# Performance work log

Hardware: AMD Instinct MI355X
Metric: run time of the kernel (lower is better)

## Reference

```python
import jax, jax.numpy as jnp
import numpy as np

NUM_EXPERT = 16
IN_FEAT = 1024
OUT_FEAT = 2048
N_TOKENS = 4096


def setup_inputs() -> dict:
    key = jax.random.key(0)
    k1, k2, k3 = jax.random.split(key, 3)
    x = jax.random.uniform(k1, (N_TOKENS, IN_FEAT), dtype=jnp.float32)
    gate = jax.random.randint(k2, (N_TOKENS,), 0, NUM_EXPERT, dtype=jnp.int32)
    # expert weights: [num_expert, out_feat, in_feat]
    weight = jax.random.normal(k3, (NUM_EXPERT, OUT_FEAT, IN_FEAT), dtype=jnp.float32) * 0.02
    return {"x": x, "gate": gate, "weight": weight}


def reference(x, gate, weight):
    # out[b] = weight[gate[b]] @ x[b]
    # Avoid materializing weight[gate] ([B, O, I] would be huge): scan over the
    # small, fixed expert axis with input masking (tokens not routed to expert e
    # contribute zero rows to that expert's GEMM).
    B = x.shape[0]
    E, O, I = weight.shape
    out0 = jnp.zeros((B, O), dtype=x.dtype)

    def body(out, ew):
        e, W = ew  # W: [O, I]
        xm = jnp.where((gate == e)[:, None], x, 0.0)  # [B, I] masked tokens
        return out + jnp.einsum("bi,oi->bo", xm, W), None

    out, _ = jax.lax.scan(body, out0, (jnp.arange(E), weight))
    return out
```

## Files before the change

kernel.cpp:

```cpp
#include <hip/hip_runtime.h>
#include <hip/hip_bf16.h>
#include <stdint.h>

#define N_TOKENS   4096
#define IN_FEAT    1024
#define OUT_FEAT   2048
#define NUM_EXPERT 16

#define BM 128
#define BN 128
#define BK 32
#define MAX_TILES 48
#define MAX_ROWS  6144

typedef __bf16 bf16x8 __attribute__((ext_vector_type(8)));
typedef float  f32x4  __attribute__((ext_vector_type(4)));
typedef unsigned short us8 __attribute__((ext_vector_type(8)));

__device__ __forceinline__ unsigned short f32_to_bf16_rne(float f) {
  union { float f; uint32_t u; } v; v.f = f;
  uint32_t u = v.u;
  u += 0x7fffu + ((u >> 16) & 1u);
  return (unsigned short)(u >> 16);
}

__device__ __forceinline__ void async_copy16(const void* g, void* l) {
  __builtin_amdgcn_global_load_lds(
      (const __attribute__((address_space(1))) unsigned int*)g,
      (__attribute__((address_space(3))) unsigned int*)l, 16, 0, 0);
}

__global__ void k_setup(const int* __restrict__ gate,
                        int* __restrict__ pstart,
                        int* __restrict__ tile_e,
                        int* __restrict__ tile_m,
                        int* __restrict__ row_token)
{
  __shared__ int cnt[NUM_EXPERT];
  __shared__ int cur[NUM_EXPERT];
  __shared__ int ps[NUM_EXPERT];
  const int tid = threadIdx.x;
  if (tid < NUM_EXPERT) { cnt[tid] = 0; cur[tid] = 0; }
  __syncthreads();
  for (int b = tid; b < N_TOKENS; b += 256) atomicAdd(&cnt[gate[b]], 1);
  for (int r = tid; r < MAX_ROWS; r += 256) row_token[r] = -1;
  __syncthreads();
  if (tid == 0) {
    int p = 0, tot = 0;
    for (int e = 0; e < NUM_EXPERT; ++e) {
      ps[e] = p; pstart[e] = p;
      int nt = (cnt[e] + BM - 1) / BM;
      for (int t = 0; t < nt; ++t) { tile_e[tot] = e; tile_m[tot] = t; ++tot; }
      p += nt * BM;
    }
    for (int s = tot; s < MAX_TILES; ++s) { tile_e[s] = -1; tile_m[s] = 0; }
  }
  __syncthreads();
  for (int b = tid; b < N_TOKENS; b += 256) {
    int e = gate[b];
    int pos = atomicAdd(&cur[e], 1);
    row_token[ps[e] + pos] = b;
  }
}

__global__ void k_gather_x(const float4* __restrict__ x,
                           const int* __restrict__ row_token,
                           us8* __restrict__ xs) {
  const int r = blockIdx.x * 2 + (threadIdx.x >> 7);
  const int c = threadIdx.x & 127;
  const int tok = row_token[r];
  us8 o;
  if (tok >= 0) {
    float4 a = x[tok * 256 + c * 2];
    float4 b = x[tok * 256 + c * 2 + 1];
    o[0] = f32_to_bf16_rne(a.x); o[1] = f32_to_bf16_rne(a.y);
    o[2] = f32_to_bf16_rne(a.z); o[3] = f32_to_bf16_rne(a.w);
    o[4] = f32_to_bf16_rne(b.x); o[5] = f32_to_bf16_rne(b.y);
    o[6] = f32_to_bf16_rne(b.z); o[7] = f32_to_bf16_rne(b.w);
  } else {
    o = (us8)0;
  }
  xs[r * 128 + c] = o;
}

__global__ void __launch_bounds__(256)
k_gemm(const unsigned short* __restrict__ xs,
       const float* __restrict__ w,
       const int* __restrict__ pstart,
       const int* __restrict__ tile_e,
       const int* __restrict__ tile_m,
       const int* __restrict__ row_token,
       float* __restrict__ out) {
  __shared__ us8   As[512];
  __shared__ f32x4 Bs[1024];
  __shared__ int rowtok_s[BM];

  const int slot = blockIdx.y;
  const int e = tile_e[slot];
  if (e < 0) return;
  const int seg0 = pstart[e] + tile_m[slot] * BM;
  const int n0 = blockIdx.x * BN;

  const int tid  = threadIdx.x;
  const int wid  = tid >> 6;
  const int lane = tid & 63;
  const int lr   = lane & 15;
  const int quad = lane >> 4;
  const int wm   = (wid >> 1) * 64;
  const int wn   = (wid & 1) * 64;

  if (tid < BM) rowtok_s[tid] = row_token[seg0 + tid];

  const int cA = (tid & 3) ^ ((tid >> 3) & 3);
  const int cB = (tid & 7) ^ ((tid >> 3) & 7);
  const unsigned short* agp = xs + (size_t)(seg0 + (tid >> 2)) * IN_FEAT + cA * 8;
  const float* bgp = w + (size_t)e * OUT_FEAT * IN_FEAT
                       + (size_t)(n0 + (tid >> 3)) * IN_FEAT + cB * 4;

  f32x4 acc[4][4];
  const f32x4 z = {0.f, 0.f, 0.f, 0.f};
#pragma unroll
  for (int i = 0; i < 4; ++i)
#pragma unroll
    for (int j = 0; j < 4; ++j) acc[i][j] = z;

  for (int k0 = 0; k0 < IN_FEAT; k0 += BK) {
    async_copy16(agp + k0,                 As + wid * 64);
    async_copy16(agp + 64 * IN_FEAT + k0,  As + 256 + wid * 64);
    async_copy16(bgp + k0,                 Bs + wid * 64);
    async_copy16(bgp + 32 * IN_FEAT + k0,  Bs + 256 + wid * 64);
    async_copy16(bgp + 64 * IN_FEAT + k0,  Bs + 512 + wid * 64);
    async_copy16(bgp + 96 * IN_FEAT + k0,  Bs + 768 + wid * 64);
    __syncthreads();

    bf16x8 af[4], bf[4];
#pragma unroll
    for (int mi = 0; mi < 4; ++mi) {
      const int n = wm + mi * 16 + lr;
      af[mi] = *(const bf16x8*)&As[n * 4 + (quad ^ ((n >> 1) & 3))];
    }
#pragma unroll
    for (int ni = 0; ni < 4; ++ni) {
      const int n = wn + ni * 16 + lr;
      f32x4 c0 = Bs[n * 8 + ((2 * quad)     ^ (n & 7))];
      f32x4 c1 = Bs[n * 8 + ((2 * quad + 1) ^ (n & 7))];
      bf16x8 b;
      b[0] = (__bf16)c0[0]; b[1] = (__bf16)c0[1];
      b[2] = (__bf16)c0[2]; b[3] = (__bf16)c0[3];
      b[4] = (__bf16)c1[0]; b[5] = (__bf16)c1[1];
      b[6] = (__bf16)c1[2]; b[7] = (__bf16)c1[3];
      bf[ni] = b;
    }
#pragma unroll
    for (int mi = 0; mi < 4; ++mi)
#pragma unroll
      for (int ni = 0; ni < 4; ++ni)
        acc[mi][ni] = __builtin_amdgcn_mfma_f32_16x16x32_bf16(
            af[mi], bf[ni], acc[mi][ni], 0, 0, 0);
    __syncthreads();
  }

#pragma unroll
  for (int mi = 0; mi < 4; ++mi) {
    const int mb = wm + mi * 16 + quad * 4;
    const int t0 = rowtok_s[mb + 0];
    const int t1 = rowtok_s[mb + 1];
    const int t2 = rowtok_s[mb + 2];
    const int t3 = rowtok_s[mb + 3];
#pragma unroll
    for (int ni = 0; ni < 4; ++ni) {
      const int n = n0 + wn + ni * 16 + lr;
      f32x4 c = acc[mi][ni];
      if (t0 >= 0) out[(size_t)t0 * OUT_FEAT + n] = c[0];
      if (t1 >= 0) out[(size_t)t1 * OUT_FEAT + n] = c[1];
      if (t2 >= 0) out[(size_t)t2 * OUT_FEAT + n] = c[2];
      if (t3 >= 0) out[(size_t)t3 * OUT_FEAT + n] = c[3];
    }
  }
}

extern "C" void kernel_launch(void* const* d_in, const int* in_sizes, int n_in,
                              void* d_out, int out_size, void* d_ws, size_t ws_size,
                              hipStream_t stream) {
  const float* x    = (const float*)d_in[0];
  const int*   gate = (const int*)d_in[1];
  const float* w    = (const float*)d_in[2];
  float* out = (float*)d_out;

  char* ws = (char*)d_ws;
  unsigned short* xs = (unsigned short*)ws;
  int* row_token = (int*)(ws + 12582912);
  int* pstart = row_token + MAX_ROWS;
  int* tile_e = pstart + NUM_EXPERT;
  int* tile_m = tile_e + MAX_TILES;

  k_setup<<<1, 256, 0, stream>>>(gate, pstart, tile_e, tile_m, row_token);
  k_gather_x<<<MAX_ROWS / 2, 256, 0, stream>>>((const float4*)x, row_token,
                                               (us8*)xs);
  dim3 g(OUT_FEAT / BN, MAX_TILES);
  k_gemm<<<g, 256, 0, stream>>>(xs, w, pstart, tile_e, tile_m, row_token, out);
}
```

Before: 260.5 us.

## Double-buffer LDS tiles in expert GEMM to overlap global loads with MFMA

The GEMM main loop now uses two LDS buffers for the A and B tiles. It issues the async global-to-LDS copies for the next K-step before computing on the current one, and waits with explicit vmcnt counts and raw s_barrier instead of __syncthreads. The goal is to hide global memory latency behind the bf16 MFMA work. The cost is double the shared memory, which can lower occupancy, and hand-written waitcnt logic that depends on the exact count of outstanding loads.

```diff
diff --git a/kernel.cpp b/kernel.cpp
--- a/kernel.cpp
+++ b/kernel.cpp
@@ -10,6 +10,7 @@
 #define BM 128
 #define BN 128
 #define BK 32
+#define NT (IN_FEAT / BK)
 #define MAX_TILES 48
 #define MAX_ROWS  6144
 
@@ -91,8 +92,8 @@
        const int* __restrict__ tile_m,
        const int* __restrict__ row_token,
        float* __restrict__ out) {
-  __shared__ us8   As[512];
-  __shared__ f32x4 Bs[1024];
+  __shared__ us8   As[2][512];
+  __shared__ f32x4 Bs[2][1024];
   __shared__ int rowtok_s[BM];
 
   const int slot = blockIdx.y;
@@ -124,26 +125,43 @@
 #pragma unroll
     for (int j = 0; j < 4; ++j) acc[i][j] = z;
 
-  for (int k0 = 0; k0 < IN_FEAT; k0 += BK) {
-    async_copy16(agp + k0,                 As + wid * 64);
-    async_copy16(agp + 64 * IN_FEAT + k0,  As + 256 + wid * 64);
-    async_copy16(bgp + k0,                 Bs + wid * 64);
-    async_copy16(bgp + 32 * IN_FEAT + k0,  Bs + 256 + wid * 64);
-    async_copy16(bgp + 64 * IN_FEAT + k0,  Bs + 512 + wid * 64);
-    async_copy16(bgp + 96 * IN_FEAT + k0,  Bs + 768 + wid * 64);
-    __syncthreads();
+  auto stage = [&](int t, int b) {
+    const int k0 = t * BK;
+    async_copy16(agp + k0,                 As[b] + wid * 64);
+    async_copy16(agp + 64 * IN_FEAT + k0,  As[b] + 256 + wid * 64);
+    async_copy16(bgp + k0,                 Bs[b] + wid * 64);
+    async_copy16(bgp + 32 * IN_FEAT + k0,  Bs[b] + 256 + wid * 64);
+    async_copy16(bgp + 64 * IN_FEAT + k0,  Bs[b] + 512 + wid * 64);
+    async_copy16(bgp + 96 * IN_FEAT + k0,  Bs[b] + 768 + wid * 64);
+  };
+
+  stage(0, 0);
+
+  asm volatile("s_waitcnt lgkmcnt(0)" ::: "memory");
+  __builtin_amdgcn_s_barrier();
+
+  for (int t = 0; t < NT; ++t) {
+    const int buf = t & 1;
+    if (t + 1 < NT) {
+      stage(t + 1, buf ^ 1);
+      asm volatile("s_waitcnt vmcnt(6)" ::: "memory");
+    } else {
+      asm volatile("s_waitcnt vmcnt(0)" ::: "memory");
+    }
+    __builtin_amdgcn_s_barrier();
+    asm volatile("" ::: "memory");
 
     bf16x8 af[4], bf[4];
 #pragma unroll
     for (int mi = 0; mi < 4; ++mi) {
       const int n = wm + mi * 16 + lr;
-      af[mi] = *(const bf16x8*)&As[n * 4 + (quad ^ ((n >> 1) & 3))];
+      af[mi] = *(const bf16x8*)&As[buf][n * 4 + (quad ^ ((n >> 1) & 3))];
     }
 #pragma unroll
     for (int ni = 0; ni < 4; ++ni) {
       const int n = wn + ni * 16 + lr;
-      f32x4 c0 = Bs[n * 8 + ((2 * quad)     ^ (n & 7))];
-      f32x4 c1 = Bs[n * 8 + ((2 * quad + 1) ^ (n & 7))];
+      f32x4 c0 = Bs[buf][n * 8 + ((2 * quad)     ^ (n & 7))];
+      f32x4 c1 = Bs[buf][n * 8 + ((2 * quad + 1) ^ (n & 7))];
       bf16x8 b;
       b[0] = (__bf16)c0[0]; b[1] = (__bf16)c0[1];
       b[2] = (__bf16)c0[2]; b[3] = (__bf16)c0[3];
@@ -157,7 +175,9 @@
       for (int ni = 0; ni < 4; ++ni)
         acc[mi][ni] = __builtin_amdgcn_mfma_f32_16x16x32_bf16(
             af[mi], bf[ni], acc[mi][ni], 0, 0, 0);
-    __syncthreads();
+
+    asm volatile("" ::: "memory");
+    __builtin_amdgcn_s_barrier();
   }
 
 #pragma unroll
```

New measurement: 260.3 us. No clear change (-0.1%).

## Make weight slice LDS-resident per block and stream token rows from global

Applied to the files above, without the earlier changes.

Restructures the grouped GEMM so each block owns one expert and a 64-column window of outputs. It loads that weight slice once, converts it to bf16 and keeps it resident in LDS for the whole K dimension. Each of 8 waves then walks 64-row chunks of the expert's tokens, reading activations directly from global memory with no per-k barriers. The aim is to remove the repeated fp32 weight reloads and in-loop conversion across M tiles. The cost is uncoalesced, unshared A loads from global, fewer blocks (16x32) and load imbalance when an expert has few chunks.

```diff
diff --git a/kernel.cpp b/kernel.cpp
--- a/kernel.cpp
+++ b/kernel.cpp
@@ -8,9 +8,8 @@
 #define NUM_EXPERT 16
 
 #define BM 128
-#define BN 128
 #define BK 32
-#define MAX_TILES 48
+#define BNW 64
 #define MAX_ROWS  6144
 
 typedef __bf16 bf16x8 __attribute__((ext_vector_type(8)));
@@ -24,16 +23,8 @@
   return (unsigned short)(u >> 16);
 }
 
-__device__ __forceinline__ void async_copy16(const void* g, void* l) {
-  __builtin_amdgcn_global_load_lds(
-      (const __attribute__((address_space(1))) unsigned int*)g,
-      (__attribute__((address_space(3))) unsigned int*)l, 16, 0, 0);
-}
-
 __global__ void k_setup(const int* __restrict__ gate,
                         int* __restrict__ pstart,
-                        int* __restrict__ tile_e,
-                        int* __restrict__ tile_m,
                         int* __restrict__ row_token)
 {
   __shared__ int cnt[NUM_EXPERT];
@@ -46,14 +37,12 @@
   for (int r = tid; r < MAX_ROWS; r += 256) row_token[r] = -1;
   __syncthreads();
   if (tid == 0) {
-    int p = 0, tot = 0;
+    int p = 0;
     for (int e = 0; e < NUM_EXPERT; ++e) {
       ps[e] = p; pstart[e] = p;
-      int nt = (cnt[e] + BM - 1) / BM;
-      for (int t = 0; t < nt; ++t) { tile_e[tot] = e; tile_m[tot] = t; ++tot; }
-      p += nt * BM;
+      p += ((cnt[e] + BM - 1) / BM) * BM;
     }
-    for (int s = tot; s < MAX_TILES; ++s) { tile_e[s] = -1; tile_m[s] = 0; }
+    pstart[NUM_EXPERT] = p;
   }
   __syncthreads();
   for (int b = tid; b < N_TOKENS; b += 256) {
@@ -83,98 +72,95 @@
   xs[r * 128 + c] = o;
 }
 
-__global__ void __launch_bounds__(256)
+__global__ void __launch_bounds__(512, 2)
 k_gemm(const unsigned short* __restrict__ xs,
        const float* __restrict__ w,
        const int* __restrict__ pstart,
-       const int* __restrict__ tile_e,
-       const int* __restrict__ tile_m,
        const int* __restrict__ row_token,
        float* __restrict__ out) {
-  __shared__ us8   As[512];
-  __shared__ f32x4 Bs[1024];
-  __shared__ int rowtok_s[BM];
+  __shared__ us8 Bs[BNW * 128];
 
-  const int slot = blockIdx.y;
-  const int e = tile_e[slot];
-  if (e < 0) return;
-  const int seg0 = pstart[e] + tile_m[slot] * BM;
-  const int n0 = blockIdx.x * BN;
+  const int e    = blockIdx.x;
+  const int nwin = blockIdx.y * BNW;
+  const int seg0 = pstart[e];
+  const int seg_len = pstart[e + 1] - seg0;
+  if (seg_len <= 0) return;
 
   const int tid  = threadIdx.x;
   const int wid  = tid >> 6;
   const int lane = tid & 63;
   const int lr   = lane & 15;
   const int quad = lane >> 4;
-  const int wm   = (wid >> 1) * 64;
-  const int wn   = (wid & 1) * 64;
 
-  if (tid < BM) rowtok_s[tid] = row_token[seg0 + tid];
+  {
+    const int n  = tid >> 3;
+    const int c8 = tid & 7;
+    const float* wp = w + (size_t)e * OUT_FEAT * IN_FEAT
+                        + (size_t)(nwin + n) * IN_FEAT;
+#pragma unroll
+    for (int p = 0; p < 16; ++p) {
+      const int c = p * 8 + c8;
+      const float4 a = *(const float4*)(wp + c * 8);
+      const float4 b = *(const float4*)(wp + c * 8 + 4);
+      us8 o;
+      o[0] = f32_to_bf16_rne(a.x); o[1] = f32_to_bf16_rne(a.y);
+      o[2] = f32_to_bf16_rne(a.z); o[3] = f32_to_bf16_rne(a.w);
+      o[4] = f32_to_bf16_rne(b.x); o[5] = f32_to_bf16_rne(b.y);
+      o[6] = f32_to_bf16_rne(b.z); o[7] = f32_to_bf16_rne(b.w);
+      Bs[n * 128 + (c ^ (n & 7))] = o;
+    }
+  }
+  __syncthreads();
 
-  const int cA = (tid & 3) ^ ((tid >> 3) & 3);
-  const int cB = (tid & 7) ^ ((tid >> 3) & 7);
-  const unsigned short* agp = xs + (size_t)(seg0 + (tid >> 2)) * IN_FEAT + cA * 8;
-  const float* bgp = w + (size_t)e * OUT_FEAT * IN_FEAT
-                       + (size_t)(n0 + (tid >> 3)) * IN_FEAT + cB * 4;
+  const int nch = seg_len >> 6;
 
-  f32x4 acc[4][4];
-  const f32x4 z = {0.f, 0.f, 0.f, 0.f};
+  for (int ch = wid; ch < nch; ch += 8) {
+    const int r0 = ch * 64;
+    const unsigned short* ap =
+        xs + (size_t)(seg0 + r0 + lr) * IN_FEAT + quad * 8;
+
+    f32x4 acc[4][4];
+    const f32x4 z = {0.f, 0.f, 0.f, 0.f};
 #pragma unroll
-  for (int i = 0; i < 4; ++i)
+    for (int i = 0; i < 4; ++i)
 #pragma unroll
-    for (int j = 0; j < 4; ++j) acc[i][j] = z;
+      for (int j = 0; j < 4; ++j) acc[i][j] = z;
 
-  for (int k0 = 0; k0 < IN_FEAT; k0 += BK) {
-    async_copy16(agp + k0,                 As + wid * 64);
-    async_copy16(agp + 64 * IN_FEAT + k0,  As + 256 + wid * 64);
-    async_copy16(bgp + k0,                 Bs + wid * 64);
-    async_copy16(bgp + 32 * IN_FEAT + k0,  Bs + 256 + wid * 64);
-    async_copy16(bgp + 64 * IN_FEAT + k0,  Bs + 512 + wid * 64);
-    async_copy16(bgp + 96 * IN_FEAT + k0,  Bs + 768 + wid * 64);
-    __syncthreads();
+#pragma unroll 4
+    for (int k0 = 0; k0 < IN_FEAT; k0 += BK) {
+      bf16x8 af[4], bf[4];
+#pragma unroll
+      for (int mi = 0; mi < 4; ++mi)
+        af[mi] = *(const bf16x8*)(ap + (size_t)mi * 16 * IN_FEAT + k0);
+#pragma unroll
+      for (int ni = 0; ni < 4; ++ni) {
+        const int n = ni * 16 + lr;
+        bf[ni] = *(const bf16x8*)&Bs[n * 128 + ((k0 / 8 + quad) ^ (n & 7))];
+      }
+#pragma unroll
+      for (int mi = 0; mi < 4; ++mi)
+#pragma unroll
+        for (int ni = 0; ni < 4; ++ni)
+          acc[mi][ni] = __builtin_amdgcn_mfma_f32_16x16x32_bf16(
+              af[mi], bf[ni], acc[mi][ni], 0, 0, 0);
+    }
 
-    bf16x8 af[4], bf[4];
 #pragma unroll
     for (int mi = 0; mi < 4; ++mi) {
-      const int n = wm + mi * 16 + lr;
-      af[mi] = *(const bf16x8*)&As[n * 4 + (quad ^ ((n >> 1) & 3))];
-    }
+      const int mb = r0 + mi * 16 + quad * 4;
+      const int t0 = row_token[seg0 + mb + 0];
+      const int t1 = row_token[seg0 + mb + 1];
+      const int t2 = row_token[seg0 + mb + 2];
+      const int t3 = row_token[seg0 + mb + 3];
 #pragma unroll
-    for (int ni = 0; ni < 4; ++ni) {
-      const int n = wn + ni * 16 + lr;
-      f32x4 c0 = Bs[n * 8 + ((2 * quad)     ^ (n & 7))];
-      f32x4 c1 = Bs[n * 8 + ((2 * quad + 1) ^ (n & 7))];
-      bf16x8 b;
-      b[0] = (__bf16)c0[0]; b[1] = (__bf16)c0[1];
-      b[2] = (__bf16)c0[2]; b[3] = (__bf16)c0[3];
-      b[4] = (__bf16)c1[0]; b[5] = (__bf16)c1[1];
-      b[6] = (__bf16)c1[2]; b[7] = (__bf16)c1[3];
-      bf[ni] = b;
-    }
-#pragma unroll
-    for (int mi = 0; mi < 4; ++mi)
-#pragma unroll
-      for (int ni = 0; ni < 4; ++ni)
-        acc[mi][ni] = __builtin_amdgcn_mfma_f32_16x16x32_bf16(
-            af[mi], bf[ni], acc[mi][ni], 0, 0, 0);
-    __syncthreads();
-  }
-
-#pragma unroll
-  for (int mi = 0; mi < 4; ++mi) {
-    const int mb = wm + mi * 16 + quad * 4;
-    const int t0 = rowtok_s[mb + 0];
-    const int t1 = rowtok_s[mb + 1];
-    const int t2 = rowtok_s[mb + 2];
-    const int t3 = rowtok_s[mb + 3];
-#pragma unroll
-    for (int ni = 0; ni < 4; ++ni) {
-      const int n = n0 + wn + ni * 16 + lr;
-      f32x4 c = acc[mi][ni];
-      if (t0 >= 0) out[(size_t)t0 * OUT_FEAT + n] = c[0];
-      if (t1 >= 0) out[(size_t)t1 * OUT_FEAT + n] = c[1];
-      if (t2 >= 0) out[(size_t)t2 * OUT_FEAT + n] = c[2];
-      if (t3 >= 0) out[(size_t)t3 * OUT_FEAT + n] = c[3];
+      for (int ni = 0; ni < 4; ++ni) {
+        const int n = nwin + ni * 16 + lr;
+        f32x4 c = acc[mi][ni];
+        if (t0 >= 0) out[(size_t)t0 * OUT_FEAT + n] = c[0];
+        if (t1 >= 0) out[(size_t)t1 * OUT_FEAT + n] = c[1];
+        if (t2 >= 0) out[(size_t)t2 * OUT_FEAT + n] = c[2];
+        if (t3 >= 0) out[(size_t)t3 * OUT_FEAT + n] = c[3];
+      }
     }
   }
 }
@@ -191,12 +177,10 @@
   unsigned short* xs = (unsigned short*)ws;
   int* row_token = (int*)(ws + 12582912);
   int* pstart = row_token + MAX_ROWS;
-  int* tile_e = pstart + NUM_EXPERT;
-  int* tile_m = tile_e + MAX_TILES;
 
-  k_setup<<<1, 256, 0, stream>>>(gate, pstart, tile_e, tile_m, row_token);
+  k_setup<<<1, 256, 0, stream>>>(gate, pstart, row_token);
   k_gather_x<<<MAX_ROWS / 2, 256, 0, stream>>>((const float4*)x, row_token,
                                                (us8*)xs);
-  dim3 g(OUT_FEAT / BN, MAX_TILES);
-  k_gemm<<<g, 256, 0, stream>>>(xs, w, pstart, tile_e, tile_m, row_token, out);
+  dim3 g(NUM_EXPERT, OUT_FEAT / BNW);
+  k_gemm<<<g, 512, 0, stream>>>(xs, w, pstart, row_token, out);
 }
```

Result: slower. 279.9 us (+7.5%).
